# Kernel tuning notes

Measured on AMD Instinct MI355X. Metric: run time of the kernel, lower is better.

Reference implementation:

```python
import jax, jax.numpy as jnp
import numpy as np

D = 512       # input_embedding_dimensions
H = 2         # num_heads
HD = D // H   # head_dim = 256
B = 16
S = 1194      # max_sequence_length


def setup_inputs() -> dict:
    key = jax.random.key(0)
    k1, k2, k3, k4, k5 = jax.random.split(key, 5)
    scale_in = 1.0 / np.sqrt(D)
    return {
        "positional_embeddings": jax.random.normal(k1, (B, S, D), dtype=jnp.float32),
        "W_qkv": jax.random.uniform(k2, (D, 3 * D), minval=-scale_in, maxval=scale_in, dtype=jnp.float32),
        "b_qkv": jax.random.uniform(k3, (3 * D,), minval=-scale_in, maxval=scale_in, dtype=jnp.float32),
        "W_out": jax.random.uniform(k4, (D, D), minval=-scale_in, maxval=scale_in, dtype=jnp.float32),
        "b_out": jax.random.uniform(k5, (D,), minval=-scale_in, maxval=scale_in, dtype=jnp.float32),
    }


def reference(positional_embeddings, W_qkv, b_qkv, W_out, b_out):
    x = positional_embeddings              # [B, S, D]
    b, s, _ = x.shape
    qkv = x @ W_qkv + b_qkv                # [B, S, 3D]
    q, k, v = jnp.split(qkv, 3, axis=-1)

    def split_heads(t):
        return t.reshape(b, s, H, HD).transpose(0, 2, 1, 3)  # [B, H, S, HD]

    q, k, v = split_heads(q), split_heads(k), split_heads(v)
    scores = jnp.einsum("bhqd,bhkd->bhqk", q, k) / jnp.sqrt(jnp.float32(HD))
    causal = jnp.tril(jnp.ones((s, s), dtype=bool))          # [S, S]
    scores = jnp.where(causal[None, None, :, :], scores, -jnp.inf)
    att = jax.nn.softmax(scores, axis=-1)                    # [B, H, S, S]
    out = jnp.einsum("bhqk,bhkd->bhqd", att, v)              # [B, H, S, HD]
    out = out.transpose(0, 2, 1, 3).reshape(b, s, D)         # [B, S, D]
    return out @ W_out + b_out
```

## Files before the change

kernel.cpp:

```cpp
#include <hip/hip_runtime.h>
#include <stdint.h>

#define D_    512
#define H_    2
#define HD_   256
#define B_    16
#define S_    1194
#define MTOK  19104
#define MPAD  19200
#define SPAD  1216
#define NQKV  1536
#define NKT   38
#define LOG2E 1.44269504088896340736f

typedef unsigned short u16;
typedef __attribute__((ext_vector_type(8))) short bf16x8;
typedef __attribute__((ext_vector_type(4))) float f32x4;

__device__ inline u16 f2bf(float x) {
  union { float f; unsigned u; } c; c.f = x;
  unsigned r = c.u + 0x7fffu + ((c.u >> 16) & 1u);
  return (u16)(r >> 16);
}

__device__ inline void async_copy16(void* lds, const void* g) {
  __builtin_amdgcn_global_load_lds(
      (__attribute__((address_space(1))) void*)(g),
      (__attribute__((address_space(3))) void*)(lds),
      16, 0, 0);
}

__global__ void convert_kernel(const float* __restrict__ X,
                               const float* __restrict__ Wqkv,
                               const float* __restrict__ Wout,
                               u16* __restrict__ Xf,
                               u16* __restrict__ Wqf,
                               u16* __restrict__ Wof) {
  const int NXG = MPAD * 64;
  const int NQG = 12 * 8 * 16 * 64;
  const int NOG = 4 * 8 * 16 * 64;
  const int TOT = NXG + NQG + NOG;
  int stride = gridDim.x * blockDim.x;
  for (int g = blockIdx.x * blockDim.x + threadIdx.x; g < TOT; g += stride) {
    if (g < NXG) {
      int lane = g & 63, f = (g >> 6) & 15, kt = (g >> 10) & 7, mt = g >> 13;
      int i = mt * 128 + (f & 7) * 16 + (lane & 15);
      int k = kt * 64 + (f >> 3) * 32 + (lane >> 4) * 8;
      bf16x8 o;
      if (i < MTOK) {
        f32x4 v0 = *(const f32x4*)&X[(size_t)i * 512 + k];
        f32x4 v1 = *(const f32x4*)&X[(size_t)i * 512 + k + 4];
#pragma unroll
        for (int e = 0; e < 4; ++e) { o[e] = (short)f2bf(v0[e]); o[4 + e] = (short)f2bf(v1[e]); }
      } else {
#pragma unroll
        for (int e = 0; e < 8; ++e) o[e] = 0;
      }
      *(bf16x8*)&Xf[(size_t)g * 8] = o;
    } else if (g < NXG + NQG) {
      int gg = g - NXG;
      int lane = gg & 63, f = (gg >> 6) & 15, kt = (gg >> 10) & 7, nt = gg >> 13;
      int j = nt * 128 + (f & 7) * 16 + (lane & 15);
      int k = kt * 64 + (f >> 3) * 32 + (lane >> 4) * 8;
      bf16x8 o;
#pragma unroll
      for (int e = 0; e < 8; ++e) o[e] = (short)f2bf(Wqkv[(size_t)(k + e) * NQKV + j]);
      *(bf16x8*)&Wqf[(size_t)gg * 8] = o;
    } else {
      int gg = g - NXG - NQG;
      int lane = gg & 63, f = (gg >> 6) & 15, kt = (gg >> 10) & 7, nt = gg >> 13;
      int j = nt * 128 + (f & 7) * 16 + (lane & 15);
      int k = kt * 64 + (f >> 3) * 32 + (lane >> 4) * 8;
      bf16x8 o;
#pragma unroll
      for (int e = 0; e < 8; ++e) o[e] = (short)f2bf(Wout[(size_t)(k + e) * 512 + j]);
      *(bf16x8*)&Wof[(size_t)gg * 8] = o;
    }
  }
}

template<int MODE>
__global__ __launch_bounds__(256, 2) void gemm_kernel(
    const u16* __restrict__ Af, const u16* __restrict__ Bf,
    const float* __restrict__ bias, int nb,
    u16* __restrict__ Qb, u16* __restrict__ Kf, u16* __restrict__ Vf,
    float* __restrict__ Cout)
{
  __shared__ u16 ldsA[2][16 * 512];
  __shared__ u16 ldsB[2][16 * 512];

  const int t  = threadIdx.x;
  const int l  = t & 63;
  const int w  = t >> 6;
  const int lr = l >> 4, lc = l & 15;

  const int nwg = gridDim.x;
  const int qq = nwg >> 3, rr8 = nwg & 7;
  const int xcd = blockIdx.x & 7, off = blockIdx.x >> 3;
  const int wgid = (xcd < rr8 ? xcd * (qq + 1) : rr8 * (qq + 1) + (xcd - rr8) * qq) + off;
  const int m0 = (wgid / nb) * 128;
  const int n0 = (wgid % nb) * 128;

  const u16* pA = Af + ((size_t)(m0 >> 7) * 128 + w) * 512 + l * 8;
  const u16* pB = Bf + ((size_t)(n0 >> 7) * 128 + w) * 512 + l * 8;

  f32x4 acc[4][4] = {};

#pragma unroll
  for (int c = 0; c < 4; ++c) {
    async_copy16(&ldsA[0][(c * 4 + w) * 512], pA + c * 2048);
    async_copy16(&ldsB[0][(c * 4 + w) * 512], pB + c * 2048);
  }
  __syncthreads();

  for (int kt = 0; kt < 8; ++kt) {
    const int cur = kt & 1;
    if (kt < 7) {
      const u16* qA = pA + (kt + 1) * 8192;
      const u16* qB = pB + (kt + 1) * 8192;
#pragma unroll
      for (int c = 0; c < 4; ++c) {
        async_copy16(&ldsA[cur ^ 1][(c * 4 + w) * 512], qA + c * 2048);
        async_copy16(&ldsB[cur ^ 1][(c * 4 + w) * 512], qB + c * 2048);
      }
    }
#pragma unroll
    for (int kk = 0; kk < 2; ++kk) {
      bf16x8 af[4], bfr[4];
#pragma unroll
      for (int m = 0; m < 4; ++m)
        af[m] = *(bf16x8*)&ldsA[cur][((kk * 8 + (w >> 1) * 4 + m) * 64 + l) * 8];
#pragma unroll
      for (int n = 0; n < 4; ++n)
        bfr[n] = *(bf16x8*)&ldsB[cur][((kk * 8 + (w & 1) * 4 + n) * 64 + l) * 8];
      __builtin_amdgcn_s_setprio(1);
#pragma unroll
      for (int m = 0; m < 4; ++m)
#pragma unroll
        for (int n = 0; n < 4; ++n)
          acc[m][n] = __builtin_amdgcn_mfma_f32_16x16x32_bf16(af[m], bfr[n], acc[m][n], 0, 0, 0);
      __builtin_amdgcn_s_setprio(0);
    }
    __syncthreads();
  }

  int jv[4]; float bj[4];
#pragma unroll
  for (int n = 0; n < 4; ++n) { jv[n] = n0 + (w & 1) * 64 + n * 16 + lc; bj[n] = bias[jv[n]]; }

#pragma unroll
  for (int m = 0; m < 4; ++m) {
#pragma unroll
    for (int r = 0; r < 4; ++r) {
      int i = m0 + (w >> 1) * 64 + m * 16 + lr * 4 + r;
      if (i >= MTOK) continue;
      if (MODE == 0) {
        int b = i / S_, s = i - b * S_;
        int stK  = s >> 5;
        int nfs  = (s >> 4) & 1;
        int lisK = s & 15;
        int lvhi = (s >> 3) & 3;
        int es   = s & 7;
#pragma unroll
        for (int n = 0; n < 4; ++n) {
          int j = jv[n];
          int which = j >> 9, h = (j >> 8) & 1, d = j & 255;
          int bh = b * H_ + h;
          u16 v = f2bf(acc[m][n][r] + bj[n]);
          if (which == 0) {
            Qb[((size_t)(bh * SPAD + s)) * HD_ + d] = v;
          } else if (which == 1) {
            Kf[(((size_t)(bh * NKT + stK)) * 16 + (d >> 5) * 2 + nfs) * 512 +
               (((d >> 3) & 3) * 16 + lisK) * 8 + (d & 7)] = v;
          } else {
            Vf[(((size_t)(bh * NKT + stK)) * 16 + (d >> 4)) * 512 +
               (lvhi * 16 + (d & 15)) * 8 + es] = v;
          }
        }
      } else {
#pragma unroll
        for (int n = 0; n < 4; ++n)
          Cout[(size_t)i * D_ + jv[n]] = acc[m][n][r] + bj[n];
      }
    }
  }
}

__global__ __launch_bounds__(256, 2) void attn_kernel(
    const u16* __restrict__ Qb, const u16* __restrict__ Kf,
    const u16* __restrict__ Vf, u16* __restrict__ Obf)
{
  __shared__ u16 ldsK[2][16 * 512];
  __shared__ u16 ldsP[4][16 * 36];

  const int id   = blockIdx.x;
  const int xcd  = id & 7;
  const int slot = id >> 3;
  const int bh   = xcd + 8 * (slot / 19);
  const int qt   = 18 - (slot % 19);
  const int q0   = qt * 64;
  const int nkv  = 2 * qt + 2;
  const int t  = threadIdx.x, l = t & 63, w = t >> 6;
  const int lr = l >> 4, lc = l & 15;
  const int wq0 = q0 + w * 16;

  bf16x8 qf[8];
  const u16* qbase = Qb + (size_t)(bh * SPAD + wq0 + lc) * HD_ + lr * 8;
#pragma unroll
  for (int kb = 0; kb < 8; ++kb)
    qf[kb] = *(const bf16x8*)(qbase + kb * 32);

  f32x4 oacc[16] = {};
  float mrow[4] = {-1e30f, -1e30f, -1e30f, -1e30f};
  float lsum[4] = {0.f, 0.f, 0.f, 0.f};

  {
    const u16* kb_ = Kf + (((size_t)(bh * NKT)) * 16 + w) * 512 + l * 8;
#pragma unroll
    for (int c = 0; c < 4; ++c)
      async_copy16(&ldsK[0][(c * 4 + w) * 512], kb_ + c * 2048);
  }
  __syncthreads();

  for (int kt = 0; kt < nkv; ++kt) {
    const int cur = kt & 1;

    bf16x8 vfr[16];
    {
      const u16* vb_ = Vf + (((size_t)(bh * NKT + kt)) * 16) * 512 + l * 8;
#pragma unroll
      for (int nf = 0; nf < 16; ++nf)
        vfr[nf] = *(const bf16x8*)(vb_ + nf * 512);
    }

    if (kt + 1 < nkv) {
      const u16* kb_ = Kf + (((size_t)(bh * NKT + kt + 1)) * 16 + w) * 512 + l * 8;
#pragma unroll
      for (int c = 0; c < 4; ++c)
        async_copy16(&ldsK[cur ^ 1][(c * 4 + w) * 512], kb_ + c * 2048);
    }

    f32x4 sacc[2] = {};
    __builtin_amdgcn_s_setprio(1);
#pragma unroll
    for (int kb = 0; kb < 8; ++kb) {
#pragma unroll
      for (int nf = 0; nf < 2; ++nf) {
        bf16x8 kf = *(bf16x8*)&ldsK[cur][((kb * 2 + nf) * 64 + l) * 8];
        sacc[nf] = __builtin_amdgcn_mfma_f32_16x16x32_bf16(qf[kb], kf, sacc[nf], 0, 0, 0);
      }
    }
    __builtin_amdgcn_s_setprio(0);

    const int kv0 = kt * 32;
    float sval[2][4];
    float pm[4] = {-1e30f, -1e30f, -1e30f, -1e30f};
    if (kv0 + 31 <= wq0) {
#pragma unroll
      for (int nf = 0; nf < 2; ++nf)
#pragma unroll
        for (int r = 0; r < 4; ++r) {
          float v = sacc[nf][r] * 0.0625f;
          sval[nf][r] = v;
          pm[r] = fmaxf(pm[r], v);
        }
    } else {
#pragma unroll
      for (int nf = 0; nf < 2; ++nf) {
        int col = kv0 + nf * 16 + lc;
#pragma unroll
        for (int r = 0; r < 4; ++r) {
          int row = wq0 + lr * 4 + r;
          float v = ((col <= row) && (col < S_)) ? sacc[nf][r] * 0.0625f : -1e30f;
          sval[nf][r] = v;
          pm[r] = fmaxf(pm[r], v);
        }
      }
    }
#pragma unroll
    for (int r = 0; r < 4; ++r) {
      pm[r] = fmaxf(pm[r], __shfl_xor(pm[r], 1));
      pm[r] = fmaxf(pm[r], __shfl_xor(pm[r], 2));
      pm[r] = fmaxf(pm[r], __shfl_xor(pm[r], 4));
      pm[r] = fmaxf(pm[r], __shfl_xor(pm[r], 8));
    }
    bool skip = (pm[0] <= mrow[0] + 8.0f) && (pm[1] <= mrow[1] + 8.0f) &&
                (pm[2] <= mrow[2] + 8.0f) && (pm[3] <= mrow[3] + 8.0f);
    if (!__all(skip)) {
#pragma unroll
      for (int r = 0; r < 4; ++r) {
        float mn = fmaxf(mrow[r], pm[r]);
        float sc = exp2f((mrow[r] - mn) * LOG2E);
        mrow[r] = mn;
        lsum[r] *= sc;
#pragma unroll
        for (int nf = 0; nf < 16; ++nf) oacc[nf][r] *= sc;
      }
    }
#pragma unroll
    for (int nf = 0; nf < 2; ++nf)
#pragma unroll
      for (int r = 0; r < 4; ++r) {
        float p = exp2f((sval[nf][r] - mrow[r]) * LOG2E);
        lsum[r] += p;
        ldsP[w][(lr * 4 + r) * 36 + nf * 16 + lc] = f2bf(p);
      }

    bf16x8 pf = *(bf16x8*)&ldsP[w][lc * 36 + lr * 8];
    __builtin_amdgcn_s_setprio(1);
#pragma unroll
    for (int nf = 0; nf < 16; ++nf)
      oacc[nf] = __builtin_amdgcn_mfma_f32_16x16x32_bf16(pf, vfr[nf], oacc[nf], 0, 0, 0);
    __builtin_amdgcn_s_setprio(0);
    __syncthreads();
  }

  float inv[4];
#pragma unroll
  for (int r = 0; r < 4; ++r) {
    float s = lsum[r];
    s += __shfl_xor(s, 1); s += __shfl_xor(s, 2);
    s += __shfl_xor(s, 4); s += __shfl_xor(s, 8);
    inv[r] = 1.0f / s;
  }
  const int b = bh >> 1, h = bh & 1;
#pragma unroll
  for (int r = 0; r < 4; ++r) {
    int qrow = wq0 + lr * 4 + r;
    if (qrow < S_) {
      int i = b * S_ + qrow;
      int it = i >> 7, mf = (i >> 4) & 7, li = i & 15;
#pragma unroll
      for (int nf = 0; nf < 16; ++nf) {
        int j = h * HD_ + nf * 16 + lc;
        size_t addr = (((size_t)(it * 8 + (j >> 6))) * 16 + ((j >> 5) & 1) * 8 + mf) * 512 +
                      (((j >> 3) & 3) * 16 + li) * 8 + (j & 7);
        Obf[addr] = f2bf(oacc[nf][r] * inv[r]);
      }
    }
  }
}

extern "C" void kernel_launch(void* const* d_in, const int* in_sizes, int n_in,
                              void* d_out, int out_size, void* d_ws, size_t ws_size,
                              hipStream_t stream) {
  const float* X    = (const float*)d_in[0];
  const float* Wqkv = (const float*)d_in[1];
  const float* bqkv = (const float*)d_in[2];
  const float* Wout = (const float*)d_in[3];
  const float* bout = (const float*)d_in[4];
  float* out = (float*)d_out;

  char* ws = (char*)d_ws;
  u16* Xf  = (u16*)ws;  ws += (size_t)MPAD * D_ * 2;
  u16* Wqf = (u16*)ws;  ws += (size_t)NQKV * D_ * 2;
  u16* Wof = (u16*)ws;  ws += (size_t)D_ * D_ * 2;
  u16* Qb  = (u16*)ws;  ws += (size_t)B_ * H_ * SPAD * HD_ * 2;
  u16* Kf  = (u16*)ws;  ws += (size_t)B_ * H_ * SPAD * HD_ * 2;
  u16* Vf  = (u16*)ws;  ws += (size_t)B_ * H_ * SPAD * HD_ * 2;
  u16* Obf = (u16*)ws;  ws += (size_t)MPAD * D_ * 2;

  convert_kernel<<<2048, 256, 0, stream>>>(X, Wqkv, Wout, Xf, Wqf, Wof);
  gemm_kernel<0><<<1800, 256, 0, stream>>>(Xf, Wqf, bqkv, 12, Qb, Kf, Vf, nullptr);
  attn_kernel<<<608, 256, 0, stream>>>(Qb, Kf, Vf, Obf);
  gemm_kernel<1><<<600, 256, 0, stream>>>(Obf, Wof, bout, 4, nullptr, nullptr, nullptr, out);
}
```

Before: 178.5 us.

## Transpose attention MFMAs so each lane owns one query row

Swaps the MFMA operand order for both QK^T and PV so the accumulator holds S^T and O^T, giving each lane a single query row. The online-softmax max and sum reductions drop from four 16-lane shuffle trees per row to two shuffles on one scalar. P is written to LDS as packed 64-bit stores instead of scalar u16 stores, and the output writes now walk head-dim within a lane. The block barrier is moved to between the P store and the P load, and the end-of-iteration barrier is removed, which may open a race on the double-buffered K tile and on ldsP across iterations.

New measurement: 165.9 us. 7.0% less time.

```diff
diff --git a/kernel.cpp b/kernel.cpp
--- a/kernel.cpp
+++ b/kernel.cpp
@@ -203,16 +203,16 @@
   const int t  = threadIdx.x, l = t & 63, w = t >> 6;
   const int lr = l >> 4, lc = l & 15;
   const int wq0 = q0 + w * 16;
+  const int qrow_l = wq0 + lc;
 
   bf16x8 qf[8];
-  const u16* qbase = Qb + (size_t)(bh * SPAD + wq0 + lc) * HD_ + lr * 8;
+  const u16* qbase = Qb + (size_t)(bh * SPAD + qrow_l) * HD_ + lr * 8;
 #pragma unroll
   for (int kb = 0; kb < 8; ++kb)
     qf[kb] = *(const bf16x8*)(qbase + kb * 32);
 
   f32x4 oacc[16] = {};
-  float mrow[4] = {-1e30f, -1e30f, -1e30f, -1e30f};
-  float lsum[4] = {0.f, 0.f, 0.f, 0.f};
+  float mrow = -1e30f, lsum = 0.f;
 
   {
     const u16* kb_ = Kf + (((size_t)(bh * NKT)) * 16 + w) * 512 + l * 8;
@@ -247,95 +247,88 @@
 #pragma unroll
       for (int nf = 0; nf < 2; ++nf) {
         bf16x8 kf = *(bf16x8*)&ldsK[cur][((kb * 2 + nf) * 64 + l) * 8];
-        sacc[nf] = __builtin_amdgcn_mfma_f32_16x16x32_bf16(qf[kb], kf, sacc[nf], 0, 0, 0);
+        sacc[nf] = __builtin_amdgcn_mfma_f32_16x16x32_bf16(kf, qf[kb], sacc[nf], 0, 0, 0);
       }
     }
     __builtin_amdgcn_s_setprio(0);
 
     const int kv0 = kt * 32;
-    float sval[2][4];
-    float pm[4] = {-1e30f, -1e30f, -1e30f, -1e30f};
+    float sv[2][4];
+    float pm = -1e30f;
     if (kv0 + 31 <= wq0) {
 #pragma unroll
       for (int nf = 0; nf < 2; ++nf)
 #pragma unroll
         for (int r = 0; r < 4; ++r) {
           float v = sacc[nf][r] * 0.0625f;
-          sval[nf][r] = v;
-          pm[r] = fmaxf(pm[r], v);
+          sv[nf][r] = v;
+          pm = fmaxf(pm, v);
         }
     } else {
 #pragma unroll
-      for (int nf = 0; nf < 2; ++nf) {
-        int col = kv0 + nf * 16 + lc;
+      for (int nf = 0; nf < 2; ++nf)
 #pragma unroll
         for (int r = 0; r < 4; ++r) {
-          int row = wq0 + lr * 4 + r;
-          float v = ((col <= row) && (col < S_)) ? sacc[nf][r] * 0.0625f : -1e30f;
-          sval[nf][r] = v;
-          pm[r] = fmaxf(pm[r], v);
+          int kv = kv0 + nf * 16 + lr * 4 + r;
+          float v = ((kv <= qrow_l) && (kv < S_)) ? sacc[nf][r] * 0.0625f : -1e30f;
+          sv[nf][r] = v;
+          pm = fmaxf(pm, v);
         }
-      }
-    }
-#pragma unroll
-    for (int r = 0; r < 4; ++r) {
-      pm[r] = fmaxf(pm[r], __shfl_xor(pm[r], 1));
-      pm[r] = fmaxf(pm[r], __shfl_xor(pm[r], 2));
-      pm[r] = fmaxf(pm[r], __shfl_xor(pm[r], 4));
-      pm[r] = fmaxf(pm[r], __shfl_xor(pm[r], 8));
-    }
-    bool skip = (pm[0] <= mrow[0] + 8.0f) && (pm[1] <= mrow[1] + 8.0f) &&
-                (pm[2] <= mrow[2] + 8.0f) && (pm[3] <= mrow[3] + 8.0f);
+    }
+    pm = fmaxf(pm, __shfl_xor(pm, 16));
+    pm = fmaxf(pm, __shfl_xor(pm, 32));
+
+    bool skip = (pm <= mrow + 8.0f);
     if (!__all(skip)) {
-#pragma unroll
-      for (int r = 0; r < 4; ++r) {
-        float mn = fmaxf(mrow[r], pm[r]);
-        float sc = exp2f((mrow[r] - mn) * LOG2E);
-        mrow[r] = mn;
-        lsum[r] *= sc;
-#pragma unroll
-        for (int nf = 0; nf < 16; ++nf) oacc[nf][r] *= sc;
-      }
-    }
-#pragma unroll
-    for (int nf = 0; nf < 2; ++nf)
-#pragma unroll
-      for (int r = 0; r < 4; ++r) {
-        float p = exp2f((sval[nf][r] - mrow[r]) * LOG2E);
-        lsum[r] += p;
-        ldsP[w][(lr * 4 + r) * 36 + nf * 16 + lc] = f2bf(p);
-      }
+      float mn = fmaxf(mrow, pm);
+      float sc = exp2f((mrow - mn) * LOG2E);
+      mrow = mn;
+      lsum *= sc;
+#pragma unroll
+      for (int nf = 0; nf < 16; ++nf)
+#pragma unroll
+        for (int r = 0; r < 4; ++r) oacc[nf][r] *= sc;
+    }
+
+#pragma unroll
+    for (int nf = 0; nf < 2; ++nf) {
+      float p0 = exp2f((sv[nf][0] - mrow) * LOG2E);
+      float p1 = exp2f((sv[nf][1] - mrow) * LOG2E);
+      float p2 = exp2f((sv[nf][2] - mrow) * LOG2E);
+      float p3 = exp2f((sv[nf][3] - mrow) * LOG2E);
+      lsum += (p0 + p1) + (p2 + p3);
+      uint64_t pk = (uint64_t)f2bf(p0) | ((uint64_t)f2bf(p1) << 16) |
+                    ((uint64_t)f2bf(p2) << 32) | ((uint64_t)f2bf(p3) << 48);
+      *(uint64_t*)&ldsP[w][lc * 36 + nf * 16 + lr * 4] = pk;
+    }
+
+    __syncthreads();
 
     bf16x8 pf = *(bf16x8*)&ldsP[w][lc * 36 + lr * 8];
     __builtin_amdgcn_s_setprio(1);
 #pragma unroll
     for (int nf = 0; nf < 16; ++nf)
-      oacc[nf] = __builtin_amdgcn_mfma_f32_16x16x32_bf16(pf, vfr[nf], oacc[nf], 0, 0, 0);
+      oacc[nf] = __builtin_amdgcn_mfma_f32_16x16x32_bf16(vfr[nf], pf, oacc[nf], 0, 0, 0);
     __builtin_amdgcn_s_setprio(0);
-    __syncthreads();
-  }
-
-  float inv[4];
-#pragma unroll
-  for (int r = 0; r < 4; ++r) {
-    float s = lsum[r];
-    s += __shfl_xor(s, 1); s += __shfl_xor(s, 2);
-    s += __shfl_xor(s, 4); s += __shfl_xor(s, 8);
-    inv[r] = 1.0f / s;
-  }
+  }
+
+  float s = lsum;
+  s += __shfl_xor(s, 16);
+  s += __shfl_xor(s, 32);
+  float inv = 1.0f / s;
+
   const int b = bh >> 1, h = bh & 1;
-#pragma unroll
-  for (int r = 0; r < 4; ++r) {
-    int qrow = wq0 + lr * 4 + r;
-    if (qrow < S_) {
-      int i = b * S_ + qrow;
-      int it = i >> 7, mf = (i >> 4) & 7, li = i & 15;
-#pragma unroll
-      for (int nf = 0; nf < 16; ++nf) {
-        int j = h * HD_ + nf * 16 + lc;
+  if (qrow_l < S_) {
+    int i = b * S_ + qrow_l;
+    int it = i >> 7, mf = (i >> 4) & 7, li = i & 15;
+#pragma unroll
+    for (int nf = 0; nf < 16; ++nf) {
+#pragma unroll
+      for (int r = 0; r < 4; ++r) {
+        int j = h * HD_ + nf * 16 + lr * 4 + r;
         size_t addr = (((size_t)(it * 8 + (j >> 6))) * 16 + ((j >> 5) & 1) * 8 + mf) * 512 +
                       (((j >> 3) & 3) * 16 + li) * 8 + (j & 7);
-        Obf[addr] = f2bf(oacc[nf][r] * inv[r]);
+        Obf[addr] = f2bf(oacc[nf][r] * inv);
       }
     }
   }
```
